# Kernel optimization log

Hardware: AMD Instinct MI355X
Metric: run time of the kernel (lower is better)

The kernel has to match this reference:

```python
import jax, jax.numpy as jnp
import numpy as np

EPS = 1e-6

def _rms_norm(x, w):
    # normalize over last dim (head_dim)
    var = jnp.mean(jnp.square(x), axis=-1, keepdims=True)
    return x * jax.lax.rsqrt(var + EPS) * w

def _rotate_half(x):
    half = x.shape[-1] // 2
    first, second = x[..., :half], x[..., half:]
    return jnp.concatenate([-second, first], axis=-1)

def _apply_rope(x, cos, sin):
    # x: [B,H,S,D]; cos/sin: [B,S,D] -> broadcast over heads
    return x * cos[:, None] + _rotate_half(x) * sin[:, None]

def setup_inputs() -> dict:
    key = jax.random.key(0)
    ks = jax.random.split(key, 10)
    B, Sq, Sk, Dm, H = 2, 2048, 2048, 2048, 16
    hd = Dm // H
    scale = 1.0 / np.sqrt(Dm)
    return {
        "x": jax.random.normal(ks[0], (B, Sq, Dm), jnp.float32),
        "context": jax.random.normal(ks[1], (B, Sk, Dm), jnp.float32),
        "cos_q": jax.random.uniform(ks[2], (B, Sq, hd), jnp.float32),
        "sin_q": jax.random.uniform(ks[3], (B, Sq, hd), jnp.float32),
        "cos_k": jax.random.uniform(ks[4], (B, Sk, hd), jnp.float32),
        "sin_k": jax.random.uniform(ks[5], (B, Sk, hd), jnp.float32),
        "Wq": jax.random.normal(ks[6], (Dm, Dm), jnp.float32) * scale,
        "Wk": jax.random.normal(ks[7], (Dm, Dm), jnp.float32) * scale,
        "Wv": jax.random.normal(ks[8], (Dm, Dm), jnp.float32) * scale,
        "Wo": jax.random.normal(ks[9], (Dm, Dm), jnp.float32) * scale,
        "q_norm_w": jnp.ones((hd,), jnp.float32),
        "k_norm_w": jnp.ones((hd,), jnp.float32),
    }

def reference(x, context, cos_q, sin_q, cos_k, sin_k, Wq, Wk, Wv, Wo, q_norm_w, k_norm_w):
    B, Sq, Dm = x.shape
    hd = q_norm_w.shape[0]
    H = Dm // hd
    # projections (torch Linear: y = x @ W.T), reshape to [B,H,S,D]
    q = (x @ Wq.T).reshape(B, Sq, H, hd).transpose(0, 2, 1, 3)
    k = (context @ Wk.T).reshape(B, -1, H, hd).transpose(0, 2, 1, 3)
    v = (context @ Wv.T).reshape(B, -1, H, hd).transpose(0, 2, 1, 3)
    # per-head QK RMSNorm
    q = _rms_norm(q, q_norm_w)
    k = _rms_norm(k, k_norm_w)
    # RoPE
    q = _apply_rope(q, cos_q, sin_q)
    k = _apply_rope(k, cos_k, sin_k)
    # SDPA, scale = 1/sqrt(head_dim)
    scale = 1.0 / np.sqrt(hd).astype(np.float32)
    scores = jnp.einsum('bhqd,bhkd->bhqk', q, k) * scale
    attn = jax.nn.softmax(scores, axis=-1)
    y = jnp.einsum('bhqk,bhkd->bhqd', attn, v)
    y = y.transpose(0, 2, 1, 3).reshape(B, Sq, Dm)
    return y @ Wo.T
```

## Files before the change

kernel.cpp:

```cpp
#include <hip/hip_runtime.h>


typedef __attribute__((ext_vector_type(8))) short bf16x8;
typedef __attribute__((ext_vector_type(4))) float f32x4;

#define AS1(p) ((__attribute__((address_space(1))) void*)(p))
#define AS3(p) ((__attribute__((address_space(3))) void*)(p))
#define STG(g, l) __builtin_amdgcn_global_load_lds(AS1(g), AS3(l), 16, 0, 0)

__device__ __forceinline__ unsigned short f2bf(float f) {
  unsigned int u = __float_as_uint(f);
  u += 0x7fffu + ((u >> 16) & 1u);
  return (unsigned short)(u >> 16);
}
__device__ __forceinline__ float bf2f(unsigned short u) {
  return __uint_as_float(((unsigned int)u) << 16);
}

constexpr int B_ = 2, S_ = 2048, DM = 2048, H_ = 16, HD = 128;
constexpr int M_ = B_ * S_;

__global__ __launch_bounds__(256) void castbf(const float* __restrict__ X,
                                              unsigned short* __restrict__ Y, int n4) {
  int i = blockIdx.x * 256 + threadIdx.x;
  if (i >= n4) return;
  float4 v = ((const float4*)X)[i];
  ushort4 u;
  u.x = f2bf(v.x); u.y = f2bf(v.y); u.z = f2bf(v.z); u.w = f2bf(v.w);
  ((ushort4*)Y)[i] = u;
}

template <int BF16OUT>
__device__ __forceinline__ void gemm_core(const unsigned short* __restrict__ A,
                                          const unsigned short* __restrict__ Bw,
                                          void* __restrict__ Cv,
                                          unsigned short* lds) {
  const int tid = threadIdx.x, wave = tid >> 6, lane = tid & 63;
  const int quad = lane >> 4, l16 = lane & 15;
  const int m0 = blockIdx.x * 128, n0 = blockIdx.y * 256;
  const int wn = wave * 64;
  constexpr int NT = DM / 32;
  constexpr int SLOT = 12288;

  f32x4 acc[8][4];
#pragma unroll
  for (int f = 0; f < 8; f++)
#pragma unroll
    for (int g = 0; g < 4; g++) acc[f][g] = (f32x4){0.f, 0.f, 0.f, 0.f};

  const unsigned short* srcA[2];
  const unsigned short* srcB[4];
#pragma unroll
  for (int i = 0; i < 2; i++) {
    int c = tid + i * 256, L = c >> 3, ph = c & 7, j = ph ^ (L & 7);
    srcA[i] = A + (size_t)(m0 + L + ((j >> 2) << 6)) * DM + (j & 3) * 8;
  }
#pragma unroll
  for (int i = 0; i < 4; i++) {
    int c = tid + i * 256, L = c >> 3, ph = c & 7, j = ph ^ (L & 7);
    srcB[i] = Bw + (size_t)(n0 + L + ((j >> 2) << 7)) * DM + (j & 3) * 8;
  }

#define STAGEK(T, S)                                                           \
  { const int ko = (T) << 5; unsigned short* lb = lds + (S) * SLOT + wave * 512;\
    STG(srcA[0] + ko, lb);                                                     \
    STG(srcA[1] + ko, lb + 2048);                                              \
    STG(srcB[0] + ko, lb + 4096);                                              \
    STG(srcB[1] + ko, lb + 6144);                                              \
    STG(srcB[2] + ko, lb + 8192);                                              \
    STG(srcB[3] + ko, lb + 10240); }

  const int x8 = l16 & 7;
  const int ab0 = l16 * 64 + ((quad ^ x8)) * 8;
  const int ab1 = l16 * 64 + (((4 | quad) ^ x8)) * 8;
  const int bb  = 4096 + (wn & 64) * 64 + l16 * 64 +
                  ((((wave >> 1) << 2) | quad) ^ x8) * 8;

  STAGEK(0, 0) STAGEK(1, 1)
  asm volatile("s_waitcnt vmcnt(6)" ::: "memory");
  __builtin_amdgcn_s_barrier();

  int st = 0, s2 = 2;
  for (int t = 0; t < NT; ++t) {
    const unsigned short* ls = lds + st * SLOT;
    bf16x8 af[8], bfv[4];
#pragma unroll
    for (int f = 0; f < 4; f++) af[f]     = *(const bf16x8*)(ls + f * 1024 + ab0);
#pragma unroll
    for (int f = 0; f < 4; f++) af[f + 4] = *(const bf16x8*)(ls + f * 1024 + ab1);
#pragma unroll
    for (int g = 0; g < 4; g++) bfv[g]    = *(const bf16x8*)(ls + g * 1024 + bb);

    if (t + 2 < NT) STAGEK(t + 2, s2)
    if (t < NT - 2)       asm volatile("s_waitcnt vmcnt(6)" ::: "memory");
    else if (t == NT - 2) asm volatile("s_waitcnt vmcnt(0)" ::: "memory");
    if (t < NT - 1) __builtin_amdgcn_s_barrier();

    __builtin_amdgcn_s_setprio(1);
#pragma unroll
    for (int f = 0; f < 8; f++)
#pragma unroll
      for (int g = 0; g < 4; g++)
        acc[f][g] = __builtin_amdgcn_mfma_f32_16x16x32_bf16(af[f], bfv[g], acc[f][g], 0, 0, 0);
    __builtin_amdgcn_s_setprio(0);

    st++; if (st == 3) st = 0;
    s2++; if (s2 == 3) s2 = 0;
  }
#undef STAGEK

#pragma unroll
  for (int f = 0; f < 8; f++)
#pragma unroll
    for (int g = 0; g < 4; g++) {
      const size_t row = (size_t)(m0 + f * 16 + quad * 4);
      const int col = n0 + wn + g * 16 + l16;
      if (BF16OUT) {
        unsigned short* cp = (unsigned short*)Cv + row * DM + col;
#pragma unroll
        for (int r = 0; r < 4; r++) cp[(size_t)r * DM] = f2bf(acc[f][g][r]);
      } else {
        float* cp = (float*)Cv + row * DM + col;
#pragma unroll
        for (int r = 0; r < 4; r++) cp[(size_t)r * DM] = acc[f][g][r];
      }
    }
}

__global__ __launch_bounds__(256, 2) void gemm_qkv(const unsigned short* __restrict__ xb,
                                                   const unsigned short* __restrict__ cb,
                                                   const unsigned short* __restrict__ Wq,
                                                   const unsigned short* __restrict__ Wk,
                                                   const unsigned short* __restrict__ Wv,
                                                   unsigned short* __restrict__ Pq,
                                                   unsigned short* __restrict__ Pk,
                                                   unsigned short* __restrict__ Pv) {
  __shared__ __align__(16) unsigned short lds[3 * 12288];
  const int z = blockIdx.z;
  const unsigned short* A  = (z == 0) ? xb : cb;
  const unsigned short* Bw = (z == 0) ? Wq : (z == 1) ? Wk : Wv;
  unsigned short* C        = (z == 0) ? Pq : (z == 1) ? Pk : Pv;
  gemm_core<1>(A, Bw, C, lds);
}

__global__ __launch_bounds__(256, 2) void gemm_bt(const unsigned short* __restrict__ A,
                                                  const unsigned short* __restrict__ Bw,
                                                  float* __restrict__ C) {
  __shared__ __align__(16) unsigned short lds[3 * 12288];
  gemm_core<0>(A, Bw, C, lds);
}

__global__ __launch_bounds__(256) void normrope(const unsigned short* __restrict__ X,
                                                const float* __restrict__ Cs,
                                                const float* __restrict__ Sn,
                                                const float* __restrict__ W,
                                                unsigned short* __restrict__ Out,
                                                float scale) {
  int gw = (blockIdx.x * 256 + threadIdx.x) >> 6;
  int lane = threadIdx.x & 63;
  int h = gw & 15, bs = gw >> 4;
  int s = bs & (S_ - 1), b = bs >> 11;
  const unsigned short* xr = X + (size_t)gw * HD;
  float x0 = bf2f(xr[lane]), x1 = bf2f(xr[lane + 64]);
  float ss = x0 * x0 + x1 * x1;
#pragma unroll
  for (int off = 32; off > 0; off >>= 1) ss += __shfl_xor(ss, off);
  float rr = rsqrtf(ss * (1.0f / 128.0f) + 1e-6f);
  float n0 = x0 * rr * W[lane], n1 = x1 * rr * W[lane + 64];
  const float* cp = Cs + (size_t)bs * HD;
  const float* sp = Sn + (size_t)bs * HD;
  float o0 = (n0 * cp[lane] - n1 * sp[lane]) * scale;
  float o1 = (n1 * cp[lane + 64] + n0 * sp[lane + 64]) * scale;
  unsigned short* orow = Out + (((size_t)(b * H_ + h)) * S_ + s) * HD;
  orow[lane] = f2bf(o0);
  orow[lane + 64] = f2bf(o1);
}

__global__ __launch_bounds__(256) void vtrans(const unsigned short* __restrict__ Vf,
                                              unsigned short* __restrict__ Vt) {
  __shared__ unsigned short tile[128 * 72];
  const int tid = threadIdx.x;
  const int sc = blockIdx.x & 31;
  const int bh = blockIdx.x >> 5;
  const int b = bh >> 4, h = bh & 15;
  const int s0 = sc * 64;
#pragma unroll
  for (int it = 0; it < 4; ++it) {
    int ci = it * 256 + tid;
    int s = ci >> 4, dc = ci & 15;
    bf16x8 v = *(const bf16x8*)(Vf + ((size_t)(b * S_ + s0 + s)) * DM + h * HD + dc * 8);
    unsigned short* tp = tile + (dc * 8) * 72 + s;
#pragma unroll
    for (int e = 0; e < 8; e++) tp[e * 72] = (unsigned short)v[e];
  }
  __syncthreads();
#pragma unroll
  for (int it = 0; it < 4; ++it) {
    int cj = it * 256 + tid;
    int d = cj >> 3, scx = cj & 7;
    bf16x8 vv = *(const bf16x8*)(tile + d * 72 + scx * 8);
    *(bf16x8*)(Vt + ((size_t)bh * HD + d) * S_ + s0 + scx * 8) = vv;
  }
}

__global__ __launch_bounds__(128) void flash(const unsigned short* __restrict__ Q,
                                             const unsigned short* __restrict__ Kt,
                                             const unsigned short* __restrict__ Vt,
                                             unsigned short* __restrict__ Y) {
  __shared__ unsigned short lK[64 * HD];
  __shared__ unsigned short lV[HD * 64];
  __shared__ unsigned short lP[2 * 1024];
  const int tid = threadIdx.x, wave = tid >> 6, lane = tid & 63;
  const int quad = lane >> 4, l16 = lane & 15;
  const int qb = blockIdx.x & 31;
  const int bh = blockIdx.x >> 5;
  const int b = bh >> 4, h = bh & 15;
  const int q0 = qb * 64 + wave * 32;

  bf16x8 aq[2][4];
#pragma unroll
  for (int u = 0; u < 2; u++) {
    const unsigned short* qrow = Q + ((size_t)bh * S_ + q0 + u * 16 + l16) * HD;
#pragma unroll
    for (int t = 0; t < 4; t++) aq[u][t] = *(const bf16x8*)(qrow + t * 32 + quad * 8);
  }
  f32x4 o[2][8];
#pragma unroll
  for (int u = 0; u < 2; u++)
#pragma unroll
    for (int t = 0; t < 8; t++) o[u][t] = (f32x4){0.f, 0.f, 0.f, 0.f};
  float lsum[2][4] = {{0.f, 0.f, 0.f, 0.f}, {0.f, 0.f, 0.f, 0.f}};

  const unsigned short* kbase = Kt + (size_t)bh * S_ * HD;
  const unsigned short* vbase = Vt + (size_t)bh * HD * S_;
  unsigned short* lPw = lP + wave * 1024;
  const int mrow = quad * 4;
  const int xsl = (l16 >> 1) & 3;
  const int xsl7 = (l16 >> 1) & 7;

  for (int k0 = 0; k0 < S_; k0 += 64) {
    __syncthreads();
#pragma unroll
    for (int call = 0; call < 8; ++call) {
      int c = call * 128 + wave * 64 + lane;
      int key = c >> 4, sk = c & 15;
      int dck = sk ^ (key & 15);
      __builtin_amdgcn_global_load_lds(AS1(kbase + (size_t)(k0 + key) * HD + dck * 8),
                                       AS3(lK + (call * 128 + wave * 64) * 8), 16, 0, 0);
      int dv = c >> 3, sv = c & 7;
      int kc = sv ^ ((dv >> 1) & 7);
      __builtin_amdgcn_global_load_lds(AS1(vbase + (size_t)dv * S_ + k0 + kc * 8),
                                       AS3(lV + (call * 128 + wave * 64) * 8), 16, 0, 0);
    }
    __syncthreads();

#pragma unroll
    for (int h2 = 0; h2 < 2; ++h2) {
      f32x4 s0[2] = {(f32x4){0.f, 0.f, 0.f, 0.f}, (f32x4){0.f, 0.f, 0.f, 0.f}};
      f32x4 s1[2] = {(f32x4){0.f, 0.f, 0.f, 0.f}, (f32x4){0.f, 0.f, 0.f, 0.f}};
      {
        const unsigned short* krow0 = lK + (h2 * 32 + l16) * HD;
        const unsigned short* krow1 = krow0 + 16 * HD;
        __builtin_amdgcn_s_setprio(1);
#pragma unroll
        for (int t = 0; t < 4; t++) {
          int dcq = t * 4 + quad;
          bf16x8 kf0 = *(const bf16x8*)(krow0 + (dcq ^ l16) * 8);
          bf16x8 kf1 = *(const bf16x8*)(krow1 + (dcq ^ l16) * 8);
#pragma unroll
          for (int u = 0; u < 2; u++) {
            s0[u] = __builtin_amdgcn_mfma_f32_16x16x32_bf16(aq[u][t], kf0, s0[u], 0, 0, 0);
            s1[u] = __builtin_amdgcn_mfma_f32_16x16x32_bf16(aq[u][t], kf1, s1[u], 0, 0, 0);
          }
        }
        __builtin_amdgcn_s_setprio(0);
      }
#pragma unroll
      for (int u = 0; u < 2; u++) {
        unsigned short* lPu = lPw + u * 512;
#pragma unroll
        for (int r = 0; r < 4; r++) {
          int m = mrow + r;
          int sx = (m >> 1) & 3;
          float p0 = __expf(s0[u][r]);
          float p1 = __expf(s1[u][r]);
          lsum[u][r] += p0 + p1;
          int kc0 = l16 >> 3;
          lPu[m * 32 + ((kc0 ^ sx)) * 8 + (l16 & 7)] = f2bf(p0);
          lPu[m * 32 + (((kc0 + 2) ^ sx)) * 8 + (l16 & 7)] = f2bf(p1);
        }
      }
      bf16x8 pf[2];
#pragma unroll
      for (int u = 0; u < 2; u++)
        pf[u] = *(const bf16x8*)(lPw + u * 512 + l16 * 32 + (quad ^ xsl) * 8);
      __builtin_amdgcn_s_setprio(1);
#pragma unroll
      for (int t = 0; t < 8; t++) {
        bf16x8 vf = *(const bf16x8*)(lV + (t * 16 + l16) * 64 + ((h2 * 4 + quad) ^ xsl7) * 8);
#pragma unroll
        for (int u = 0; u < 2; u++)
          o[u][t] = __builtin_amdgcn_mfma_f32_16x16x32_bf16(pf[u], vf, o[u][t], 0, 0, 0);
      }
      __builtin_amdgcn_s_setprio(0);
    }
  }

#pragma unroll
  for (int off = 1; off < 16; off <<= 1) {
#pragma unroll
    for (int u = 0; u < 2; u++)
#pragma unroll
      for (int r = 0; r < 4; r++) lsum[u][r] += __shfl_xor(lsum[u][r], off);
  }
  float inv[2][4];
#pragma unroll
  for (int u = 0; u < 2; u++)
#pragma unroll
    for (int r = 0; r < 4; r++) inv[u][r] = 1.0f / lsum[u][r];
#pragma unroll
  for (int u = 0; u < 2; u++)
#pragma unroll
    for (int t = 0; t < 8; t++)
#pragma unroll
      for (int r = 0; r < 4; r++) {
        size_t idx = ((size_t)b * S_ + q0 + u * 16 + mrow + r) * DM + h * HD + t * 16 + l16;
        Y[idx] = f2bf(o[u][t][r] * inv[u][r]);
      }
}

extern "C" void kernel_launch(void* const* d_in, const int* in_sizes, int n_in,
                              void* d_out, int out_size, void* d_ws, size_t ws_size,
                              hipStream_t stream) {
  const float* x    = (const float*)d_in[0];
  const float* ctx  = (const float*)d_in[1];
  const float* cosq = (const float*)d_in[2];
  const float* sinq = (const float*)d_in[3];
  const float* cosk = (const float*)d_in[4];
  const float* sink = (const float*)d_in[5];
  const float* Wq   = (const float*)d_in[6];
  const float* Wk   = (const float*)d_in[7];
  const float* Wv   = (const float*)d_in[8];
  const float* Wo   = (const float*)d_in[9];
  const float* qw   = (const float*)d_in[10];
  const float* kw   = (const float*)d_in[11];

  char* ws = (char*)d_ws;
  const size_t ACT2 = (size_t)M_ * DM * 2;
  const size_t W2   = (size_t)DM * DM * 2;
  unsigned short* xb  = (unsigned short*)(ws);
  unsigned short* cb  = (unsigned short*)(ws + ACT2);
  unsigned short* Wqb = (unsigned short*)(ws + 2 * ACT2);
  unsigned short* Wkb = (unsigned short*)(ws + 2 * ACT2 + W2);
  unsigned short* Wvb = (unsigned short*)(ws + 2 * ACT2 + 2 * W2);
  unsigned short* Wob = (unsigned short*)(ws + 2 * ACT2 + 3 * W2);
  unsigned short* Pq  = (unsigned short*)(ws + 2 * ACT2 + 4 * W2);
  unsigned short* Pk  = (unsigned short*)(ws + 3 * ACT2 + 4 * W2);
  unsigned short* Pv  = (unsigned short*)(ws + 4 * ACT2 + 4 * W2);
  unsigned short* qn = xb;
  unsigned short* kn = Wqb;
  unsigned short* vt = cb;
  unsigned short* yb = Pq;

  const float scale = 0.0883883476483184f;

  castbf<<<M_ * DM / 1024, 256, 0, stream>>>(x, xb, M_ * DM / 4);
  castbf<<<M_ * DM / 1024, 256, 0, stream>>>(ctx, cb, M_ * DM / 4);
  castbf<<<DM * DM / 1024, 256, 0, stream>>>(Wq, Wqb, DM * DM / 4);
  castbf<<<DM * DM / 1024, 256, 0, stream>>>(Wk, Wkb, DM * DM / 4);
  castbf<<<DM * DM / 1024, 256, 0, stream>>>(Wv, Wvb, DM * DM / 4);
  castbf<<<DM * DM / 1024, 256, 0, stream>>>(Wo, Wob, DM * DM / 4);

  dim3 gq(M_ / 128, DM / 256, 3);
  gemm_qkv<<<gq, 256, 0, stream>>>(xb, cb, Wqb, Wkb, Wvb, Pq, Pk, Pv);

  normrope<<<M_ * H_ / 4, 256, 0, stream>>>(Pq, cosq, sinq, qw, qn, scale);
  normrope<<<M_ * H_ / 4, 256, 0, stream>>>(Pk, cosk, sink, kw, kn, 1.0f);
  vtrans<<<B_ * H_ * (S_ / 64), 256, 0, stream>>>(Pv, vt);

  flash<<<B_ * H_ * (S_ / 64), 128, 0, stream>>>(qn, kn, vt, yb);

  dim3 gg(M_ / 128, DM / 256);
  gemm_bt<<<gg, 256, 0, stream>>>(yb, Wob, (float*)d_out);

  (void)in_sizes; (void)n_in; (void)out_size; (void)ws_size;
}
```

Baseline: 478.1 us.

## Double-buffer K/V tiles in flash attention and widen blocks to four waves

The flash kernel now uses 256-thread blocks covering 128 query rows, so each staged K/V tile is shared by four waves instead of two. It double-buffers K and V in LDS, prefetching the next tile with async global-to-LDS loads while the current one is computed, and uses partial vmcnt waits with raw barriers instead of full syncthreads. The goal is to hide global load latency and halve K/V traffic per query row. In exchange LDS use rises to about 72KB per block, which limits occupancy, and correctness now depends on the hand-tuned waitcnt count.

```diff
diff --git a/kernel.cpp b/kernel.cpp
--- a/kernel.cpp
+++ b/kernel.cpp
@@ -203,19 +203,19 @@
   }
 }
 
-__global__ __launch_bounds__(128) void flash(const unsigned short* __restrict__ Q,
-                                             const unsigned short* __restrict__ Kt,
-                                             const unsigned short* __restrict__ Vt,
-                                             unsigned short* __restrict__ Y) {
-  __shared__ unsigned short lK[64 * HD];
-  __shared__ unsigned short lV[HD * 64];
-  __shared__ unsigned short lP[2 * 1024];
+__global__ __launch_bounds__(256, 2) void flash(const unsigned short* __restrict__ Q,
+                                                const unsigned short* __restrict__ Kt,
+                                                const unsigned short* __restrict__ Vt,
+                                                unsigned short* __restrict__ Y) {
+  __shared__ unsigned short lK[2 * 64 * HD];
+  __shared__ unsigned short lV[2 * HD * 64];
+  __shared__ unsigned short lP[4 * 1024];
   const int tid = threadIdx.x, wave = tid >> 6, lane = tid & 63;
   const int quad = lane >> 4, l16 = lane & 15;
-  const int qb = blockIdx.x & 31;
-  const int bh = blockIdx.x >> 5;
+  const int qb = blockIdx.x & 15;
+  const int bh = blockIdx.x >> 4;
   const int b = bh >> 4, h = bh & 15;
-  const int q0 = qb * 64 + wave * 32;
+  const int q0 = qb * 128 + wave * 32;
 
   bf16x8 aq[2][4];
 #pragma unroll
@@ -238,28 +238,44 @@
   const int xsl = (l16 >> 1) & 3;
   const int xsl7 = (l16 >> 1) & 7;
 
-  for (int k0 = 0; k0 < S_; k0 += 64) {
-    __syncthreads();
-#pragma unroll
-    for (int call = 0; call < 8; ++call) {
-      int c = call * 128 + wave * 64 + lane;
-      int key = c >> 4, sk = c & 15;
-      int dck = sk ^ (key & 15);
-      __builtin_amdgcn_global_load_lds(AS1(kbase + (size_t)(k0 + key) * HD + dck * 8),
-                                       AS3(lK + (call * 128 + wave * 64) * 8), 16, 0, 0);
-      int dv = c >> 3, sv = c & 7;
-      int kc = sv ^ ((dv >> 1) & 7);
-      __builtin_amdgcn_global_load_lds(AS1(vbase + (size_t)dv * S_ + k0 + kc * 8),
-                                       AS3(lV + (call * 128 + wave * 64) * 8), 16, 0, 0);
+#define STAGEKV(K0, BUF)                                                       \
+  {                                                                            \
+    const unsigned short* kb_ = kbase + (size_t)(K0) * HD;                     \
+    const unsigned short* vb_ = vbase + (K0);                                  \
+    _Pragma("unroll")                                                          \
+    for (int call = 0; call < 4; ++call) {                                     \
+      int c = call * 256 + tid;                         \
+      int key = c >> 4, sk = c & 15;           \
+      int dck = sk ^ (key & 15);                                               \
+      STG(kb_ + (size_t)key * HD + dck * 8,                                    \
+          lK + (BUF) * 8192 + (call * 256 + wave * 64) * 8);                   \
+      int dv = c >> 3, sv = c & 7;             \
+      int kc = sv ^ ((dv >> 1) & 7);                                           \
+      STG(vb_ + (size_t)dv * S_ + kc * 8,                                      \
+          lV + (BUF) * 8192 + (call * 256 + wave * 64) * 8);                   \
+    }                                                                          \
+  }
+
+  STAGEKV(0, 0)
+
+  for (int it = 0; it < S_ / 64; ++it) {
+    if (it + 1 < S_ / 64) {
+      STAGEKV((it + 1) * 64, (it + 1) & 1)
+      asm volatile("s_waitcnt vmcnt(8)" ::: "memory");
+    } else {
+      asm volatile("s_waitcnt vmcnt(0)" ::: "memory");
     }
-    __syncthreads();
+    __builtin_amdgcn_s_barrier();
+
+    const unsigned short* lKc = lK + (it & 1) * 8192;
+    const unsigned short* lVc = lV + (it & 1) * 8192;
 
 #pragma unroll
     for (int h2 = 0; h2 < 2; ++h2) {
       f32x4 s0[2] = {(f32x4){0.f, 0.f, 0.f, 0.f}, (f32x4){0.f, 0.f, 0.f, 0.f}};
       f32x4 s1[2] = {(f32x4){0.f, 0.f, 0.f, 0.f}, (f32x4){0.f, 0.f, 0.f, 0.f}};
       {
-        const unsigned short* krow0 = lK + (h2 * 32 + l16) * HD;
+        const unsigned short* krow0 = lKc + (h2 * 32 + l16) * HD;
         const unsigned short* krow1 = krow0 + 16 * HD;
         __builtin_amdgcn_s_setprio(1);
 #pragma unroll
@@ -297,14 +313,17 @@
       __builtin_amdgcn_s_setprio(1);
 #pragma unroll
       for (int t = 0; t < 8; t++) {
-        bf16x8 vf = *(const bf16x8*)(lV + (t * 16 + l16) * 64 + ((h2 * 4 + quad) ^ xsl7) * 8);
+        bf16x8 vf = *(const bf16x8*)(lVc + (t * 16 + l16) * 64 + ((h2 * 4 + quad) ^ xsl7) * 8);
 #pragma unroll
         for (int u = 0; u < 2; u++)
           o[u][t] = __builtin_amdgcn_mfma_f32_16x16x32_bf16(pf[u], vf, o[u][t], 0, 0, 0);
       }
       __builtin_amdgcn_s_setprio(0);
     }
-  }
+
+    __builtin_amdgcn_s_barrier();
+  }
+#undef STAGEKV
 
 #pragma unroll
   for (int off = 1; off < 16; off <<= 1) {
@@ -378,7 +397,7 @@
   normrope<<<M_ * H_ / 4, 256, 0, stream>>>(Pk, cosk, sink, kw, kn, 1.0f);
   vtrans<<<B_ * H_ * (S_ / 64), 256, 0, stream>>>(Pv, vt);
 
-  flash<<<B_ * H_ * (S_ / 64), 128, 0, stream>>>(qn, kn, vt, yb);
+  flash<<<B_ * H_ * (S_ / 128), 256, 0, stream>>>(qn, kn, vt, yb);
 
   dim3 gg(M_ / 128, DM / 256);
   gemm_bt<<<gg, 256, 0, stream>>>(yb, Wob, (float*)d_out);
```

Measured after the change: 457.4 us. 1.05x faster.
